# Performance work log

Hardware: AMD Instinct MI355X
Metric: run time of the kernel (lower is better)

Reference implementation:

```python
import jax, jax.numpy as jnp
import numpy as np

EPS = 1e-8


def _cdist(a, b):
    # Euclidean pairwise distances [N, M] via ||a||^2 + ||b||^2 - 2 a b^T
    a2 = jnp.sum(a * a, axis=-1, keepdims=True)          # [N, 1]
    b2 = jnp.sum(b * b, axis=-1, keepdims=True).T        # [1, M]
    sq = a2 + b2 - 2.0 * (a @ b.T)                       # [N, M]
    return jnp.sqrt(jnp.maximum(sq, 1e-12))


def setup_inputs() -> dict:
    key = jax.random.key(0)
    k1, k2, k3 = jax.random.split(key, 3)
    N, M = 16384, 16384
    # scale to metric-like LiDAR coordinates
    query_points = jax.random.normal(k1, (N, 3), dtype=jnp.float32) * 20.0
    ref_points = jax.random.normal(k2, (M, 3), dtype=jnp.float32) * 20.0
    ref_flow = jax.random.normal(k3, (M, 3), dtype=jnp.float32)
    return {"query_points": query_points, "ref_points": ref_points,
            "ref_flow": ref_flow, "k": 3}


def reference(query_points, ref_points, ref_flow, k):
    # knn_interpolate_flow (pure-torch fallback path), method='knn'
    dist = _cdist(query_points, ref_points)              # [N, M]
    neg_d, knn_idx = jax.lax.top_k(-dist, k)             # smallest k distances
    knn_dist = -neg_d                                    # [N, k]
    weights = 1.0 / (knn_dist + EPS)
    weights = weights / jnp.sum(weights, axis=1, keepdims=True)
    knn_flow = ref_flow[knn_idx]                         # [N, k, 3]
    interpolated_flow = jnp.sum(weights[..., None] * knn_flow, axis=1)  # [N, 3]
    return interpolated_flow
```

## Files before the change

kernel.cpp:

```cpp
#include <hip/hip_runtime.h>
#include <math.h>

#define BLOCK 256
#define QPT   4
#define CHUNK 512
#define S     64
#define DELTA 0.05f

__device__ __forceinline__ float mul_rn(float a, float b) {
#pragma clang fp contract(off)
    return a * b;
}
__device__ __forceinline__ float add_rn(float a, float b) {
#pragma clang fp contract(off)
    return a + b;
}
__device__ __forceinline__ float sumsq3(float x, float y, float z) {
    return add_rn(add_rn(mul_rn(x, x), mul_rn(y, y)), mul_rn(z, z));
}
__device__ __forceinline__ float med3f(float a, float b, float c) {
    return __builtin_amdgcn_fmed3f(a, b, c);
}
__device__ __forceinline__ float pair_sq(float a0, float a1, float a2, float an,
                                         float bx, float by, float bz, float bw) {
    const float dot = __builtin_fmaf(a2, bz,
                      __builtin_fmaf(a1, by, mul_rn(a0, bx)));
    return __builtin_fmaf(-2.0f, dot, add_rn(an, bw));
}

__device__ __forceinline__ void val3_push(float& d0, float& d1, float& d2, float v) {
    d2 = med3f(d1, d2, v);
    d1 = med3f(d0, d1, v);
    d0 = fminf(d0, v);
}

__device__ __forceinline__ void lex3_push(float& d0, float& d1, float& d2,
                                          int& i0, int& i1, int& i2,
                                          float sq, int idx) {
    const bool l0 = (sq < d0) || (sq == d0 && idx < i0);
    const bool l1 = (sq < d1) || (sq == d1 && idx < i1);
    const bool l2 = (sq < d2) || (sq == d2 && idx < i2);
    i2 = l1 ? i1 : (l2 ? idx : i2);
    d2 = l1 ? d1 : (l2 ? sq  : d2);
    i1 = l0 ? i0 : (l1 ? idx : i1);
    d1 = l0 ? d0 : (l1 ? sq  : d1);
    i0 = l0 ? idx : i0;
    d0 = l0 ? sq  : d0;
}

__device__ __forceinline__ void stage_chunk(const float* __restrict__ r,
                                            int start, int cnt,
                                            float4* __restrict__ smem) {
    const int t = threadIdx.x;
    if (t < (cnt >> 2)) {
        const float4* p = (const float4*)(r + (size_t)(start + t * 4) * 3);
        const float4 A = p[0], B = p[1], C = p[2];
        smem[t * 4 + 0] = make_float4(-2.0f * A.x, -2.0f * A.y, -2.0f * A.z,
                                      sumsq3(A.x, A.y, A.z));
        smem[t * 4 + 1] = make_float4(-2.0f * A.w, -2.0f * B.x, -2.0f * B.y,
                                      sumsq3(A.w, B.x, B.y));
        smem[t * 4 + 2] = make_float4(-2.0f * B.z, -2.0f * B.w, -2.0f * C.x,
                                      sumsq3(B.z, B.w, C.x));
        smem[t * 4 + 3] = make_float4(-2.0f * C.y, -2.0f * C.z, -2.0f * C.w,
                                      sumsq3(C.y, C.z, C.w));
    }
}

__global__ __launch_bounds__(BLOCK, 4) void values_kernel(
    const float* __restrict__ q, const float* __restrict__ r,
    float* __restrict__ smin, int N, int refsPerSlice)
{
    __shared__ float4 smem[CHUNK];
    const int tid = threadIdx.x;
    const int s   = blockIdx.y;
    const int start = s * refsPerSlice;

    float a0[QPT], a1[QPT], a2[QPT], an[QPT], d0[QPT];
#pragma unroll
    for (int u = 0; u < QPT; ++u) {
        const int qi = (blockIdx.x * QPT + u) * BLOCK + tid;
        a0[u] = q[qi * 3 + 0];
        a1[u] = q[qi * 3 + 1];
        a2[u] = q[qi * 3 + 2];
        an[u] = sumsq3(a0[u], a1[u], a2[u]);
        d0[u] = __builtin_inff();
    }

    for (int coff = 0; coff < refsPerSlice; coff += CHUNK) {
        const int cnt = min(CHUNK, refsPerSlice - coff);
        __syncthreads();
        stage_chunk(r, start + coff, cnt, smem);
        __syncthreads();
#pragma unroll 4
        for (int j = 0; j < cnt; j += 2) {
            const float4 b0 = smem[j];
            const float4 b1 = smem[j + 1];
#pragma unroll
            for (int u = 0; u < QPT; ++u) {
                const float t0 = __builtin_fmaf(a2[u], b0.z,
                                 __builtin_fmaf(a1[u], b0.y,
                                 __builtin_fmaf(a0[u], b0.x, b0.w)));
                const float t1 = __builtin_fmaf(a2[u], b1.z,
                                 __builtin_fmaf(a1[u], b1.y,
                                 __builtin_fmaf(a0[u], b1.x, b1.w)));
                d0[u] = fminf(fminf(t0, t1), d0[u]);
            }
        }
    }

#pragma unroll
    for (int u = 0; u < QPT; ++u) {
        const int qi = (blockIdx.x * QPT + u) * BLOCK + tid;
        smin[(size_t)qi * S + s] = an[u] + d0[u];
    }
}

__global__ __launch_bounds__(BLOCK, 4) void rescan_kernel(
    const float* __restrict__ q, const float* __restrict__ r,
    const float* __restrict__ smin, const float* __restrict__ flow,
    float* __restrict__ out, int N, int refsPerSlice)
{
    const int lane = threadIdx.x & 63;
    const int qi   = blockIdx.x * (BLOCK / 64) + (threadIdx.x >> 6);

    const float a0 = q[qi * 3 + 0];
    const float a1 = q[qi * 3 + 1];
    const float a2 = q[qi * 3 + 2];
    const float an = sumsq3(a0, a1, a2);

    const float v = smin[(size_t)qi * S + lane];
    float g0 = v, g1 = __builtin_inff(), g2 = __builtin_inff();
#pragma unroll
    for (int m = 1; m < 64; m <<= 1) {
        const float e0 = __shfl_xor(g0, m);
        const float e1 = __shfl_xor(g1, m);
        const float e2 = __shfl_xor(g2, m);
        val3_push(g0, g1, g2, e0);
        val3_push(g0, g1, g2, e1);
        val3_push(g0, g1, g2, e2);
    }

    unsigned long long mask = __ballot(v <= g2 + DELTA);

    float d0 = __builtin_inff(), d1 = __builtin_inff(), d2 = __builtin_inff();
    int   i0 = 0x7fffffff, i1 = 0x7fffffff, i2 = 0x7fffffff;
    const int K = refsPerSlice >> 6;

    while (mask) {
        const int s = (int)__builtin_ctzll(mask);
        mask &= mask - 1;
        const int base = s * refsPerSlice;
        for (int k = 0; k < K; ++k) {
            const int idx = base + lane + (k << 6);
            const float b0 = r[3 * idx + 0];
            const float b1 = r[3 * idx + 1];
            const float b2 = r[3 * idx + 2];
            const float bw = sumsq3(b0, b1, b2);
            const float sq = pair_sq(a0, a1, a2, an, b0, b1, b2, bw);
            const bool c0 = sq < d0;
            const bool c1 = sq < d1;
            const bool c2 = sq < d2;
            i2 = c1 ? i1 : (c2 ? idx : i2);
            d2 = c1 ? d1 : (c2 ? sq  : d2);
            i1 = c0 ? i0 : (c1 ? idx : i1);
            d1 = c0 ? d0 : (c1 ? sq  : d1);
            i0 = c0 ? idx : i0;
            d0 = c0 ? sq  : d0;
        }
    }

#pragma unroll
    for (int m = 1; m < 64; m <<= 1) {
        const float e0 = __shfl_xor(d0, m);
        const float e1 = __shfl_xor(d1, m);
        const float e2 = __shfl_xor(d2, m);
        const int   j0 = __shfl_xor(i0, m);
        const int   j1 = __shfl_xor(i1, m);
        const int   j2 = __shfl_xor(i2, m);
        lex3_push(d0, d1, d2, i0, i1, i2, e0, j0);
        lex3_push(d0, d1, d2, i0, i1, i2, e1, j1);
        lex3_push(d0, d1, d2, i0, i1, i2, e2, j2);
    }

    if (lane == 0) {
        const float t0 = sqrtf(fmaxf(d0, 1e-12f));
        const float t1 = sqrtf(fmaxf(d1, 1e-12f));
        const float t2 = sqrtf(fmaxf(d2, 1e-12f));
        const float w0r = 1.0f / add_rn(t0, 1e-8f);
        const float w1r = 1.0f / add_rn(t1, 1e-8f);
        const float w2r = 1.0f / add_rn(t2, 1e-8f);
        const float wsum = add_rn(add_rn(w0r, w1r), w2r);
        const float w0 = w0r / wsum;
        const float w1 = w1r / wsum;
        const float w2 = w2r / wsum;

        const float f00 = flow[3 * i0 + 0], f01 = flow[3 * i0 + 1], f02 = flow[3 * i0 + 2];
        const float f10 = flow[3 * i1 + 0], f11 = flow[3 * i1 + 1], f12 = flow[3 * i1 + 2];
        const float f20 = flow[3 * i2 + 0], f21 = flow[3 * i2 + 1], f22 = flow[3 * i2 + 2];

        out[qi * 3 + 0] = add_rn(add_rn(mul_rn(w0, f00), mul_rn(w1, f10)), mul_rn(w2, f20));
        out[qi * 3 + 1] = add_rn(add_rn(mul_rn(w0, f01), mul_rn(w1, f11)), mul_rn(w2, f21));
        out[qi * 3 + 2] = add_rn(add_rn(mul_rn(w0, f02), mul_rn(w1, f12)), mul_rn(w2, f22));
    }
}

extern "C" void kernel_launch(void* const* d_in, const int* in_sizes, int n_in,
                              void* d_out, int out_size, void* d_ws, size_t ws_size,
                              hipStream_t stream) {
    const float* q    = (const float*)d_in[0];
    const float* r    = (const float*)d_in[1];
    const float* flow = (const float*)d_in[2];

    const int N = in_sizes[0] / 3;
    const int M = in_sizes[1] / 3;

    const int refsPerSlice = M / S;
    float* smin = (float*)d_ws;
    (void)ws_size;

    dim3 grid1(N / (BLOCK * QPT), S);
    values_kernel<<<grid1, BLOCK, 0, stream>>>(q, r, smin, N, refsPerSlice);

    rescan_kernel<<<N / (BLOCK / 64), BLOCK, 0, stream>>>(
        q, r, smin, flow, (float*)d_out, N, refsPerSlice);
}
```

Baseline: 104.7 us.

## Precompute packed reference float4s in a prep kernel and read them directly from global

Adds a prep kernel that converts the reference points once into packed float4 (-2x, -2y, -2z, |r|^2) in workspace. The values kernel then drops its shared-memory staging and __syncthreads, and reads the uniform float4 stream straight from global memory, relying on scalar or broadcast caching. This removes the redundant per-block staging and barriers but adds a kernel launch and a pass through global memory. Because every lane reads the same address, the loads might be turned into scalar loads, though in practice they could go through the vector L1 instead.

```diff
diff --git a/kernel.cpp b/kernel.cpp
--- a/kernel.cpp
+++ b/kernel.cpp
@@ -3,7 +3,6 @@
 
 #define BLOCK 256
 #define QPT   4
-#define CHUNK 512
 #define S     64
 #define DELTA 0.05f
 
@@ -48,32 +47,30 @@
     d0 = l0 ? sq  : d0;
 }
 
-__device__ __forceinline__ void stage_chunk(const float* __restrict__ r,
-                                            int start, int cnt,
-                                            float4* __restrict__ smem) {
-    const int t = threadIdx.x;
-    if (t < (cnt >> 2)) {
-        const float4* p = (const float4*)(r + (size_t)(start + t * 4) * 3);
-        const float4 A = p[0], B = p[1], C = p[2];
-        smem[t * 4 + 0] = make_float4(-2.0f * A.x, -2.0f * A.y, -2.0f * A.z,
-                                      sumsq3(A.x, A.y, A.z));
-        smem[t * 4 + 1] = make_float4(-2.0f * A.w, -2.0f * B.x, -2.0f * B.y,
-                                      sumsq3(A.w, B.x, B.y));
-        smem[t * 4 + 2] = make_float4(-2.0f * B.z, -2.0f * B.w, -2.0f * C.x,
-                                      sumsq3(B.z, B.w, C.x));
-        smem[t * 4 + 3] = make_float4(-2.0f * C.y, -2.0f * C.z, -2.0f * C.w,
-                                      sumsq3(C.y, C.z, C.w));
-    }
+__global__ __launch_bounds__(BLOCK) void prep_kernel(
+    const float* __restrict__ r, float4* __restrict__ r4)
+{
+    const int t = blockIdx.x * BLOCK + threadIdx.x;
+    const float4* p = (const float4*)(r + (size_t)t * 12);
+    const float4 A = p[0], B = p[1], C = p[2];
+    float4* o = r4 + (size_t)t * 4;
+    o[0] = make_float4(-2.0f * A.x, -2.0f * A.y, -2.0f * A.z,
+                       sumsq3(A.x, A.y, A.z));
+    o[1] = make_float4(-2.0f * A.w, -2.0f * B.x, -2.0f * B.y,
+                       sumsq3(A.w, B.x, B.y));
+    o[2] = make_float4(-2.0f * B.z, -2.0f * B.w, -2.0f * C.x,
+                       sumsq3(B.z, B.w, C.x));
+    o[3] = make_float4(-2.0f * C.y, -2.0f * C.z, -2.0f * C.w,
+                       sumsq3(C.y, C.z, C.w));
 }
 
 __global__ __launch_bounds__(BLOCK, 4) void values_kernel(
-    const float* __restrict__ q, const float* __restrict__ r,
+    const float* __restrict__ q, const float4* __restrict__ r4,
     float* __restrict__ smin, int N, int refsPerSlice)
 {
-    __shared__ float4 smem[CHUNK];
     const int tid = threadIdx.x;
     const int s   = blockIdx.y;
-    const int start = s * refsPerSlice;
+    const float4* __restrict__ rs = r4 + (size_t)s * refsPerSlice;
 
     float a0[QPT], a1[QPT], a2[QPT], an[QPT], d0[QPT];
 #pragma unroll
@@ -86,25 +83,19 @@
         d0[u] = __builtin_inff();
     }
 
-    for (int coff = 0; coff < refsPerSlice; coff += CHUNK) {
-        const int cnt = min(CHUNK, refsPerSlice - coff);
-        __syncthreads();
-        stage_chunk(r, start + coff, cnt, smem);
-        __syncthreads();
-#pragma unroll 4
-        for (int j = 0; j < cnt; j += 2) {
-            const float4 b0 = smem[j];
-            const float4 b1 = smem[j + 1];
-#pragma unroll
-            for (int u = 0; u < QPT; ++u) {
-                const float t0 = __builtin_fmaf(a2[u], b0.z,
-                                 __builtin_fmaf(a1[u], b0.y,
-                                 __builtin_fmaf(a0[u], b0.x, b0.w)));
-                const float t1 = __builtin_fmaf(a2[u], b1.z,
-                                 __builtin_fmaf(a1[u], b1.y,
-                                 __builtin_fmaf(a0[u], b1.x, b1.w)));
-                d0[u] = fminf(fminf(t0, t1), d0[u]);
-            }
+#pragma unroll 8
+    for (int j = 0; j < refsPerSlice; j += 2) {
+        const float4 b0 = rs[j];
+        const float4 b1 = rs[j + 1];
+#pragma unroll
+        for (int u = 0; u < QPT; ++u) {
+            const float t0 = __builtin_fmaf(a2[u], b0.z,
+                             __builtin_fmaf(a1[u], b0.y,
+                             __builtin_fmaf(a0[u], b0.x, b0.w)));
+            const float t1 = __builtin_fmaf(a2[u], b1.z,
+                             __builtin_fmaf(a1[u], b1.y,
+                             __builtin_fmaf(a0[u], b1.x, b1.w)));
+            d0[u] = fminf(fminf(t0, t1), d0[u]);
         }
     }
 
@@ -215,11 +206,14 @@
     const int M = in_sizes[1] / 3;
 
     const int refsPerSlice = M / S;
-    float* smin = (float*)d_ws;
+    float*  smin = (float*)d_ws;
+    float4* r4   = (float4*)((char*)d_ws + (size_t)N * S * sizeof(float));
     (void)ws_size;
 
+    prep_kernel<<<M / (4 * BLOCK), BLOCK, 0, stream>>>(r, r4);
+
     dim3 grid1(N / (BLOCK * QPT), S);
-    values_kernel<<<grid1, BLOCK, 0, stream>>>(q, r, smin, N, refsPerSlice);
+    values_kernel<<<grid1, BLOCK, 0, stream>>>(q, r4, smin, N, refsPerSlice);
 
     rescan_kernel<<<N / (BLOCK / 64), BLOCK, 0, stream>>>(
         q, r, smin, flow, (float*)d_out, N, refsPerSlice);
```

Result: slower. 115.8 us (+10.7%).
